# Kernel optimization log

Hardware: AMD Instinct MI355X
Metric: run time of the kernel (lower is better)

## Reference

```python
import jax, jax.numpy as jnp
import numpy as np

B, L, D = 2, 2048, 2048
H, G, E = 16, 4, 128       # num_heads, group_num, head dim
KV = H // G                # kv heads = 4
OUT = D                    # output_dim == input_dim for residual


def setup_inputs() -> dict:
    key = jax.random.key(0)
    ks = jax.random.split(key, 12)
    s_in = 1.0 / np.sqrt(D)
    s_o = 1.0 / np.sqrt(H * E)
    return {
        "x": jax.random.normal(ks[0], (B, L, D), jnp.float32),
        "Wq": jax.random.normal(ks[1], (D, H * E), jnp.float32) * s_in,
        "bq": jnp.zeros((H * E,), jnp.float32),
        "Wk": jax.random.normal(ks[2], (D, KV * E), jnp.float32) * s_in,
        "bk": jnp.zeros((KV * E,), jnp.float32),
        "Wv": jax.random.normal(ks[3], (D, KV * E), jnp.float32) * s_in,
        "bv": jnp.zeros((KV * E,), jnp.float32),
        "Wo": jax.random.normal(ks[4], (H * E, OUT), jnp.float32) * s_o,
        "bo": jnp.zeros((OUT,), jnp.float32),
        "gamma": jnp.ones((OUT,), jnp.float32),
        "beta": jnp.zeros((OUT,), jnp.float32),
    }


def reference(x, Wq, bq, Wk, bk, Wv, bv, Wo, bo, gamma, beta):
    b, l, _ = x.shape
    Q = (x @ Wq + bq).reshape(b, l, H, E)            # [B,L,H,E]
    K = (x @ Wk + bk).reshape(b, l, KV, E)           # [B,L,KV,E]
    V = (x @ Wv + bv).reshape(b, l, KV, E)
    # GQA expand: reshape(B,L,1,KV,E).expand(G) -> head h = g*KV + kv (tile kv heads G times)
    K = jnp.broadcast_to(K[:, :, None, :, :], (b, l, G, KV, E)).reshape(b, l, H, E)
    V = jnp.broadcast_to(V[:, :, None, :, :], (b, l, G, KV, E)).reshape(b, l, H, E)
    scores = jnp.einsum('blhe,bmhe->bhlm', Q, K) / np.sqrt(E).astype(np.float32)
    # causal mask: triu(ones, diag=1) * -1e9 added to scores
    mask = jnp.triu(jnp.ones((l, l), jnp.float32), k=1) * (-1e9)
    attn = jax.nn.softmax(scores + mask[None, None, :, :], axis=-1)
    ctx = jnp.einsum('bhlm,bmhe->blhe', attn, V).reshape(b, l, H * E)
    y = jax.nn.gelu(ctx @ Wo + bo, approximate=False)  # nn.GELU default = exact erf
    r = x + y
    mu = jnp.mean(r, axis=-1, keepdims=True)
    var = jnp.var(r, axis=-1, keepdims=True)
    return (r - mu) * jax.lax.rsqrt(var + 1e-5) * gamma + beta
```

## Files before the change

kernel.cpp:

```cpp
#include <hip/hip_runtime.h>
#include <hip/hip_bf16.h>
#include <math.h>

typedef __bf16 bf16_t;
typedef __bf16 bf16x4 __attribute__((ext_vector_type(4)));
typedef __bf16 bf16x8 __attribute__((ext_vector_type(8)));
typedef float  f32x4  __attribute__((ext_vector_type(4)));
typedef float  f32x16 __attribute__((ext_vector_type(16)));

#define MFMA16(a,b,c) __builtin_amdgcn_mfma_f32_16x16x32_bf16((a),(b),(c),0,0,0)
#define MFMA32(a,b,c) __builtin_amdgcn_mfma_f32_32x32x16_bf16((a),(b),(c),0,0,0)

#define B_ 2
#define L_ 2048
#define D_ 2048
#define H_ 16
#define KV_ 4
#define E_ 128
#define M_ (B_*L_)
#define NQKV_ 3072

__device__ __forceinline__ void async_ld16(const bf16_t* g, bf16_t* l) {
    __builtin_amdgcn_global_load_lds((const __attribute__((address_space(1))) void*)g,
                                     (__attribute__((address_space(3))) void*)l, 16, 0, 0);
}

__global__ __launch_bounds__(256) void cast_bias_kernel(const float* __restrict__ src,
                                                        bf16_t* __restrict__ dst,
                                                        const float* __restrict__ bq,
                                                        const float* __restrict__ bk,
                                                        const float* __restrict__ bv,
                                                        float* __restrict__ qbias) {
    int bid = blockIdx.x;
    if (bid < 8192) {
        int i = (bid * 256 + threadIdx.x) * 4;
        float4 v = *(const float4*)(src + i);
        bf16x4 o;
        o.x = (bf16_t)v.x; o.y = (bf16_t)v.y; o.z = (bf16_t)v.z; o.w = (bf16_t)v.w;
        *(bf16x4*)(dst + i) = o;
    } else {
        int i = (bid - 8192) * 256 + threadIdx.x;
        if (i < 2048) qbias[i] = bq[i];
        else if (i < 2560) qbias[i] = bk[i - 2048];
        else if (i < 3072) qbias[i] = bv[i - 2560];
    }
}

__global__ __launch_bounds__(256) void wtrans_kernel(const float* __restrict__ Wq,
                                                     const float* __restrict__ Wk,
                                                     const float* __restrict__ Wv,
                                                     const float* __restrict__ Wo,
                                                     bf16_t* __restrict__ WqkvT,
                                                     bf16_t* __restrict__ WoT) {
    __shared__ float tile[32][33];
    int bx = blockIdx.x;
    const float* W; bf16_t* WT; int N, n0;
    if (bx < 64)      { W = Wq; WT = WqkvT;                  N = 2048; n0 = bx * 32; }
    else if (bx < 80) { W = Wk; WT = WqkvT + 2048 * 2048;    N = 512;  n0 = (bx - 64) * 32; }
    else if (bx < 96) { W = Wv; WT = WqkvT + 2560 * 2048;    N = 512;  n0 = (bx - 80) * 32; }
    else              { W = Wo; WT = WoT;                    N = 2048; n0 = (bx - 96) * 32; }
    int k0 = blockIdx.y * 32;
    int tx = threadIdx.x, ty = threadIdx.y;
    #pragma unroll
    for (int i = 0; i < 32; i += 8)
        tile[ty + i][tx] = W[(size_t)(k0 + ty + i) * N + n0 + tx];
    __syncthreads();
    #pragma unroll
    for (int i = 0; i < 32; i += 8)
        WT[(size_t)(n0 + ty + i) * 2048 + k0 + tx] = (bf16_t)tile[tx][ty + i];
}

__global__ __launch_bounds__(256) void transpose_v_kernel(const bf16_t* __restrict__ QKV,
                                                          bf16_t* __restrict__ Vt) {
    __shared__ bf16_t tile[32][33];
    int e0 = blockIdx.x * 32, l0 = blockIdx.y * 32;
    int bk = blockIdx.z;
    int b = bk >> 2, kv = bk & 3;
    int tx = threadIdx.x, ty = threadIdx.y;
    #pragma unroll
    for (int i = 0; i < 32; i += 8)
        tile[ty + i][tx] = QKV[(size_t)(b * L_ + l0 + ty + i) * NQKV_ + 2560 + kv * 128 + e0 + tx];
    __syncthreads();
    #pragma unroll
    for (int i = 0; i < 32; i += 8)
        Vt[((size_t)bk * 128 + e0 + ty + i) * L_ + l0 + tx] = tile[tx][ty + i];
}

template <bool OUT_BF16, bool GELU>
__global__ __launch_bounds__(256) void gemm_kernel(const bf16_t* __restrict__ A,
                                                   const bf16_t* __restrict__ BT,
                                                   const float* __restrict__ bias,
                                                   void* __restrict__ C,
                                                   int M, int N, int K) {
    __shared__ __align__(16) bf16_t sA[128][32];
    __shared__ __align__(16) bf16_t sB[128][32];
    int tid = threadIdx.x;
    int wave = tid >> 6, lane = tid & 63;
    int l16 = lane & 15, quad = lane >> 4;
    int row0 = blockIdx.y * 128;
    int col0 = blockIdx.x * 128;
    int wm = (wave >> 1) * 64;
    int wn = (wave & 1) * 64;

    f32x4 acc[4][4];
    #pragma unroll
    for (int i = 0; i < 4; ++i)
        #pragma unroll
        for (int j = 0; j < 4; ++j)
            acc[i][j] = f32x4{0.f, 0.f, 0.f, 0.f};

    for (int k0 = 0; k0 < K; k0 += 32) {
        #pragma unroll
        for (int c = 0; c < 2; ++c) {
            int lin = (c * 256 + tid) * 8;
            int r = lin >> 5, col = lin & 31;
            async_ld16(&A[(size_t)(row0 + r) * K + k0 + col], &sA[r][col]);
            async_ld16(&BT[(size_t)(col0 + r) * K + k0 + col], &sB[r][col]);
        }
        __syncthreads();
        bf16x8 af[4], bf[4];
        #pragma unroll
        for (int mt = 0; mt < 4; ++mt) af[mt] = *(const bf16x8*)&sA[wm + mt * 16 + l16][quad * 8];
        #pragma unroll
        for (int nt = 0; nt < 4; ++nt) bf[nt] = *(const bf16x8*)&sB[wn + nt * 16 + l16][quad * 8];
        #pragma unroll
        for (int mt = 0; mt < 4; ++mt)
            #pragma unroll
            for (int nt = 0; nt < 4; ++nt)
                acc[mt][nt] = MFMA16(af[mt], bf[nt], acc[mt][nt]);
        __syncthreads();
    }

    #pragma unroll
    for (int mt = 0; mt < 4; ++mt) {
        #pragma unroll
        for (int nt = 0; nt < 4; ++nt) {
            int gcol = col0 + wn + nt * 16 + l16;
            float bv = bias[gcol];
            #pragma unroll
            for (int r = 0; r < 4; ++r) {
                int grow = row0 + wm + mt * 16 + quad * 4 + r;
                float v = acc[mt][nt][r] + bv;
                if (GELU) v = 0.5f * v * (1.f + erff(v * 0.70710678118654752f));
                if (OUT_BF16) ((bf16_t*)C)[(size_t)grow * N + gcol] = (bf16_t)v;
                else          ((float*)C)[(size_t)grow * N + gcol] = v;
            }
        }
    }
}

__global__ __launch_bounds__(256) void attn_kernel(const bf16_t* __restrict__ QKV,
                                                   const bf16_t* __restrict__ Vt,
                                                   bf16_t* __restrict__ Ctx) {
    __shared__ __align__(16) bf16_t sK[2][64][128];
    __shared__ __align__(16) bf16_t sV[2][128][64];

    const int tid = threadIdx.x;
    const int wave = tid >> 6, lane = tid & 63;
    const int l31 = lane & 31, half = lane >> 5;

    const int idx = blockIdx.x;
    const int r = idx >> 5;
    const int bh = idx & 31;
    const int t = (r < 8) ? (15 - r) : (r - 8);
    const int h = bh & 15, b = bh >> 4;
    const int kv = h & 3;

    const bf16_t* Kbase = QKV + (size_t)b * L_ * NQKV_ + 2048 + kv * 128;
    const bf16_t* Vbase = Vt + (size_t)(b * 4 + kv) * 128 * L_;
    const float SC = 0.12754995f;

    const int qrow = t * 128 + wave * 32 + l31;
    const int ktlast = 2 * t + 1;
    const int ktmax_w = 2 * t + (wave >> 1);

    bf16x8 qf[8];
    const bf16_t* Qrow = QKV + (size_t)(b * L_ + qrow) * NQKV_ + h * 128 + half * 8;
    #pragma unroll
    for (int et = 0; et < 8; ++et) qf[et] = *(const bf16x8*)&Qrow[et * 16];

    f32x16 acc[4];
    #pragma unroll
    for (int em = 0; em < 4; ++em)
        #pragma unroll
        for (int j = 0; j < 16; ++j) acc[em][j] = 0.f;
    float l_i = 0.f;

    bf16x8 kreg[4], vreg[4];
    #define LOAD_TILE(KT)                                                            \
        {                                                                            \
            int kk = (KT) * 64;                                                      \
            _Pragma("unroll")                                                        \
            for (int p = 0; p < 4; ++p) {                                            \
                int ch = p * 256 + tid;                                              \
                int rk = ch >> 4, ck = ch & 15;                                      \
                kreg[p] = *(const bf16x8*)&Kbase[(size_t)(kk + rk) * NQKV_ + ck * 8];\
                int rv = ch >> 3, cv = ch & 7;                                       \
                vreg[p] = *(const bf16x8*)&Vbase[(size_t)rv * L_ + kk + cv * 8];     \
            }                                                                        \
        }

    LOAD_TILE(0);

    for (int kt = 0; kt <= ktlast; ++kt) {
        const int bufi = kt & 1;
        #pragma unroll
        for (int p = 0; p < 4; ++p) {
            int ch = p * 256 + tid;
            int rk = ch >> 4, ck = ch & 15;
            *(bf16x8*)&sK[bufi][rk][(ck ^ (rk & 15)) * 8] = kreg[p];
            int rv = ch >> 3, cv = ch & 7;
            *(bf16x8*)&sV[bufi][rv][(cv ^ (rv & 7)) * 8] = vreg[p];
        }
        __syncthreads();
        if (kt < ktlast) LOAD_TILE(kt + 1);

        if (kt <= ktmax_w) {
            f32x16 s0[2], s1[2];
            #pragma unroll
            for (int mt = 0; mt < 2; ++mt)
                #pragma unroll
                for (int j = 0; j < 16; ++j) { s0[mt][j] = 0.f; s1[mt][j] = 0.f; }
            __builtin_amdgcn_s_setprio(1);
            #pragma unroll
            for (int mt = 0; mt < 2; ++mt)
                #pragma unroll
                for (int ep = 0; ep < 4; ++ep) {
                    bf16x8 kf0 = *(const bf16x8*)&sK[bufi][mt * 32 + l31][((ep * 4 + half) ^ (l31 & 15)) * 8];
                    bf16x8 kf1 = *(const bf16x8*)&sK[bufi][mt * 32 + l31][((ep * 4 + 2 + half) ^ (l31 & 15)) * 8];
                    s0[mt] = MFMA32(kf0, qf[ep * 2], s0[mt]);
                    s1[mt] = MFMA32(kf1, qf[ep * 2 + 1], s1[mt]);
                }
            __builtin_amdgcn_s_setprio(0);
            f32x16 s[2];
            #pragma unroll
            for (int mt = 0; mt < 2; ++mt)
                #pragma unroll
                for (int j = 0; j < 16; ++j) s[mt][j] = s0[mt][j] + s1[mt][j];

            if (kt == ktmax_w) {
                #pragma unroll
                for (int mt = 0; mt < 2; ++mt)
                    #pragma unroll
                    for (int j = 0; j < 16; ++j) {
                        int kidx = kt * 64 + mt * 32 + (j & 3) + 8 * (j >> 2) + 4 * half;
                        if (kidx > qrow) s[mt][j] = -3.0e38f;
                    }
            }

            float rs = 0.f;
            #pragma unroll
            for (int mt = 0; mt < 2; ++mt)
                #pragma unroll
                for (int j = 0; j < 16; ++j) {
                    float p = exp2f(s[mt][j] * SC);
                    s[mt][j] = p;
                    rs += p;
                }
            rs += __shfl_xor(rs, 32, 64);
            l_i += rs;

            bf16x4 pk[2][4];
            #pragma unroll
            for (int mt = 0; mt < 2; ++mt)
                #pragma unroll
                for (int g = 0; g < 4; ++g) {
                    bf16x4 tt;
                    #pragma unroll
                    for (int i = 0; i < 4; ++i) tt[i] = (bf16_t)s[mt][g * 4 + i];
                    pk[mt][g] = tt;
                }

            #pragma unroll
            for (int kc = 0; kc < 4; ++kc) {
                const int mts = kc >> 1, g0 = 2 * (kc & 1);
                bf16x4 send = half ? pk[mts][g0] : pk[mts][g0 + 1];
                bf16x4 keep = half ? pk[mts][g0 + 1] : pk[mts][g0];
                union { bf16x4 v; int i[2]; } su, ru;
                su.v = send;
                ru.i[0] = __shfl_xor(su.i[0], 32, 64);
                ru.i[1] = __shfl_xor(su.i[1], 32, 64);
                bf16x4 lo = half ? ru.v : keep;
                bf16x4 hi = half ? keep : ru.v;
                bf16x8 pf = __builtin_shufflevector(lo, hi, 0, 1, 2, 3, 4, 5, 6, 7);
                __builtin_amdgcn_s_setprio(1);
                #pragma unroll
                for (int em = 0; em < 4; ++em) {
                    bf16x8 vf = *(const bf16x8*)&sV[bufi][em * 32 + l31][((kc * 2 + half) ^ (l31 & 7)) * 8];
                    acc[em] = MFMA32(vf, pf, acc[em]);
                }
                __builtin_amdgcn_s_setprio(0);
            }
        }
    }

    const float inv = 1.f / l_i;
    bf16_t* Cp = Ctx + (size_t)(b * L_ + qrow) * 2048 + h * 128;
    #pragma unroll
    for (int em = 0; em < 4; ++em)
        #pragma unroll
        for (int g = 0; g < 4; ++g) {
            bf16x4 ov;
            #pragma unroll
            for (int i = 0; i < 4; ++i) ov[i] = (bf16_t)(acc[em][g * 4 + i] * inv);
            *(bf16x4*)&Cp[em * 32 + g * 8 + half * 4] = ov;
        }
}

__global__ __launch_bounds__(256) void ln_kernel(const bf16_t* __restrict__ Y,
                                                 const float* __restrict__ X,
                                                 const float* __restrict__ gamma,
                                                 const float* __restrict__ beta,
                                                 float* __restrict__ out) {
    __shared__ float sr[2048];
    __shared__ float wred[8];
    size_t row = blockIdx.x;
    const bf16_t* y = Y + row * 2048;
    const float* x = X + row * 2048;
    float sum = 0.f, ssq = 0.f;
    #pragma unroll
    for (int c = 0; c < 2; ++c) {
        int i = (c * 256 + threadIdx.x) * 4;
        bf16x4 yv = *(const bf16x4*)(y + i);
        float4 xv = *(const float4*)(x + i);
        float r0 = xv.x + (float)yv[0];
        float r1 = xv.y + (float)yv[1];
        float r2 = xv.z + (float)yv[2];
        float r3 = xv.w + (float)yv[3];
        sr[i] = r0; sr[i + 1] = r1; sr[i + 2] = r2; sr[i + 3] = r3;
        sum += r0 + r1 + r2 + r3;
        ssq += r0 * r0 + r1 * r1 + r2 * r2 + r3 * r3;
    }
    #pragma unroll
    for (int off = 32; off > 0; off >>= 1) {
        sum += __shfl_xor(sum, off, 64);
        ssq += __shfl_xor(ssq, off, 64);
    }
    int wv = threadIdx.x >> 6;
    if ((threadIdx.x & 63) == 0) { wred[wv] = sum; wred[wv + 4] = ssq; }
    __syncthreads();
    sum = wred[0] + wred[1] + wred[2] + wred[3];
    ssq = wred[4] + wred[5] + wred[6] + wred[7];
    float mu = sum * (1.f / 2048.f);
    float var = ssq * (1.f / 2048.f) - mu * mu;
    float rstd = rsqrtf(var + 1e-5f);
    #pragma unroll
    for (int c = 0; c < 2; ++c) {
        int i = (c * 256 + threadIdx.x) * 4;
        float4 gv = *(const float4*)(gamma + i);
        float4 bv = *(const float4*)(beta + i);
        float4 o;
        o.x = (sr[i]     - mu) * rstd * gv.x + bv.x;
        o.y = (sr[i + 1] - mu) * rstd * gv.y + bv.y;
        o.z = (sr[i + 2] - mu) * rstd * gv.z + bv.z;
        o.w = (sr[i + 3] - mu) * rstd * gv.w + bv.w;
        *(float4*)(out + row * 2048 + i) = o;
    }
}

extern "C" void kernel_launch(void* const* d_in, const int* in_sizes, int n_in,
                              void* d_out, int out_size, void* d_ws, size_t ws_size,
                              hipStream_t stream) {
    const float* x     = (const float*)d_in[0];
    const float* Wq    = (const float*)d_in[1];
    const float* bq    = (const float*)d_in[2];
    const float* Wk    = (const float*)d_in[3];
    const float* bk    = (const float*)d_in[4];
    const float* Wv    = (const float*)d_in[5];
    const float* bv    = (const float*)d_in[6];
    const float* Wo    = (const float*)d_in[7];
    const float* bo    = (const float*)d_in[8];
    const float* gamma = (const float*)d_in[9];
    const float* beta  = (const float*)d_in[10];
    float* out = (float*)d_out;

    char* ws = (char*)d_ws;
    size_t off = 0;
    bf16_t* xb    = (bf16_t*)(ws + off); off += 16777216;
    bf16_t* WqkvT = (bf16_t*)(ws + off); off += 12582912;
    bf16_t* WoT   = (bf16_t*)(ws + off); off += 8388608;
    float*  qbias = (float*)(ws + off);  off += 12288;
    bf16_t* QKV   = (bf16_t*)(ws + off); off += 25165824;
    bf16_t* Vt    = (bf16_t*)(ws + off); off += 4194304;
    bf16_t* Cb    = (bf16_t*)(ws + off); off += 16777216;
    bf16_t* Yb    = (bf16_t*)(ws + off); off += 16777216;

    cast_bias_kernel<<<8204, 256, 0, stream>>>(x, xb, bq, bk, bv, qbias);
    wtrans_kernel<<<dim3(160, 64), dim3(32, 8), 0, stream>>>(Wq, Wk, Wv, Wo, WqkvT, WoT);

    gemm_kernel<true, false><<<dim3(24, 32), 256, 0, stream>>>(xb, WqkvT, qbias, QKV, M_, NQKV_, D_);
    transpose_v_kernel<<<dim3(4, 64, 8), dim3(32, 8), 0, stream>>>(QKV, Vt);
    attn_kernel<<<512, 256, 0, stream>>>(QKV, Vt, Cb);
    gemm_kernel<true, true><<<dim3(16, 32), 256, 0, stream>>>(Cb, WoT, bo, Yb, M_, D_, 2048);
    ln_kernel<<<M_, 256, 0, stream>>>(Yb, x, gamma, beta, out);
}
```

Baseline: 387.0 us.

## Restructure attention into 64-row blocks with async K staging and direct V loads

The attention kernel now runs 1024 blocks of 128 threads, each covering 64 query rows instead of 128, with a new tile ordering that pairs long and short causal rows for load balance. K tiles are staged into LDS through asynchronous global-to-LDS loads. V fragments are read straight from global memory into registers, so the V shared buffer goes away. This removes the wasted diagonal work of idle waves and the register round-trip for staging, but adds per-wave global V traffic and higher register pressure.

```diff
diff --git a/kernel.cpp b/kernel.cpp
--- a/kernel.cpp
+++ b/kernel.cpp
@@ -149,20 +149,19 @@
     }
 }
 
-__global__ __launch_bounds__(256) void attn_kernel(const bf16_t* __restrict__ QKV,
-                                                   const bf16_t* __restrict__ Vt,
-                                                   bf16_t* __restrict__ Ctx) {
+__global__ __launch_bounds__(128, 2) void attn_kernel(const bf16_t* __restrict__ QKV,
+                                                      const bf16_t* __restrict__ Vt,
+                                                      bf16_t* __restrict__ Ctx) {
     __shared__ __align__(16) bf16_t sK[2][64][128];
-    __shared__ __align__(16) bf16_t sV[2][128][64];
 
     const int tid = threadIdx.x;
     const int wave = tid >> 6, lane = tid & 63;
     const int l31 = lane & 31, half = lane >> 5;
 
     const int idx = blockIdx.x;
-    const int r = idx >> 5;
+    const int rr = idx >> 5;
     const int bh = idx & 31;
-    const int t = (r < 8) ? (15 - r) : (r - 8);
+    const int u = (rr < 8) ? 31 - rr : (rr < 16) ? rr - 8 : (rr < 24) ? 39 - rr : rr - 16;
     const int h = bh & 15, b = bh >> 4;
     const int kv = h & 3;
 
@@ -170,9 +169,7 @@
     const bf16_t* Vbase = Vt + (size_t)(b * 4 + kv) * 128 * L_;
     const float SC = 0.12754995f;
 
-    const int qrow = t * 128 + wave * 32 + l31;
-    const int ktlast = 2 * t + 1;
-    const int ktmax_w = 2 * t + (wave >> 1);
+    const int qrow = u * 64 + wave * 32 + l31;
 
     bf16x8 qf[8];
     const bf16_t* Qrow = QKV + (size_t)(b * L_ + qrow) * NQKV_ + h * 128 + half * 8;
@@ -186,112 +183,109 @@
         for (int j = 0; j < 16; ++j) acc[em][j] = 0.f;
     float l_i = 0.f;
 
-    bf16x8 kreg[4], vreg[4];
-    #define LOAD_TILE(KT)                                                            \
-        {                                                                            \
-            int kk = (KT) * 64;                                                      \
-            _Pragma("unroll")                                                        \
-            for (int p = 0; p < 4; ++p) {                                            \
-                int ch = p * 256 + tid;                                              \
-                int rk = ch >> 4, ck = ch & 15;                                      \
-                kreg[p] = *(const bf16x8*)&Kbase[(size_t)(kk + rk) * NQKV_ + ck * 8];\
-                int rv = ch >> 3, cv = ch & 7;                                       \
-                vreg[p] = *(const bf16x8*)&Vbase[(size_t)rv * L_ + kk + cv * 8];     \
-            }                                                                        \
-        }
-
-    LOAD_TILE(0);
-
-    for (int kt = 0; kt <= ktlast; ++kt) {
+    #define STAGE_K(KT, BUF)                                                          \
+        {                                                                             \
+            int kk = (KT) * 64;                                                       \
+            _Pragma("unroll")                                                         \
+            for (int rep = 0; rep < 8; ++rep) {                                       \
+                int ch = rep * 128 + tid;                                             \
+                int rk = ch >> 4;                                                     \
+                int sc = (ch & 15) ^ (rk & 15);                                       \
+                async_ld16(&Kbase[(size_t)(kk + rk) * NQKV_ + sc * 8],                \
+                           ((bf16_t*)sK[BUF]) + (size_t)ch * 8);                      \
+            }                                                                         \
+        }
+
+    STAGE_K(0, 0);
+    __syncthreads();
+
+    for (int kt = 0; kt <= u; ++kt) {
         const int bufi = kt & 1;
-        #pragma unroll
-        for (int p = 0; p < 4; ++p) {
-            int ch = p * 256 + tid;
-            int rk = ch >> 4, ck = ch & 15;
-            *(bf16x8*)&sK[bufi][rk][(ck ^ (rk & 15)) * 8] = kreg[p];
-            int rv = ch >> 3, cv = ch & 7;
-            *(bf16x8*)&sV[bufi][rv][(cv ^ (rv & 7)) * 8] = vreg[p];
-        }
-        __syncthreads();
-        if (kt < ktlast) LOAD_TILE(kt + 1);
-
-        if (kt <= ktmax_w) {
-            f32x16 s0[2], s1[2];
-            #pragma unroll
-            for (int mt = 0; mt < 2; ++mt)
-                #pragma unroll
-                for (int j = 0; j < 16; ++j) { s0[mt][j] = 0.f; s1[mt][j] = 0.f; }
-            __builtin_amdgcn_s_setprio(1);
-            #pragma unroll
-            for (int mt = 0; mt < 2; ++mt)
-                #pragma unroll
-                for (int ep = 0; ep < 4; ++ep) {
-                    bf16x8 kf0 = *(const bf16x8*)&sK[bufi][mt * 32 + l31][((ep * 4 + half) ^ (l31 & 15)) * 8];
-                    bf16x8 kf1 = *(const bf16x8*)&sK[bufi][mt * 32 + l31][((ep * 4 + 2 + half) ^ (l31 & 15)) * 8];
-                    s0[mt] = MFMA32(kf0, qf[ep * 2], s0[mt]);
-                    s1[mt] = MFMA32(kf1, qf[ep * 2 + 1], s1[mt]);
-                }
-            __builtin_amdgcn_s_setprio(0);
-            f32x16 s[2];
-            #pragma unroll
-            for (int mt = 0; mt < 2; ++mt)
-                #pragma unroll
-                for (int j = 0; j < 16; ++j) s[mt][j] = s0[mt][j] + s1[mt][j];
-
-            if (kt == ktmax_w) {
-                #pragma unroll
-                for (int mt = 0; mt < 2; ++mt)
-                    #pragma unroll
-                    for (int j = 0; j < 16; ++j) {
-                        int kidx = kt * 64 + mt * 32 + (j & 3) + 8 * (j >> 2) + 4 * half;
-                        if (kidx > qrow) s[mt][j] = -3.0e38f;
-                    }
+        if (kt < u) STAGE_K(kt + 1, bufi ^ 1);
+
+        bf16x8 vr[16];
+        #pragma unroll
+        for (int kc = 0; kc < 2; ++kc)
+            #pragma unroll
+            for (int em = 0; em < 4; ++em)
+                vr[kc * 4 + em] = *(const bf16x8*)&Vbase[(size_t)(em * 32 + l31) * L_ +
+                                                         kt * 64 + (kc * 2 + half) * 8];
+
+        f32x16 s[2];
+        #pragma unroll
+        for (int mt = 0; mt < 2; ++mt)
+            #pragma unroll
+            for (int j = 0; j < 16; ++j) s[mt][j] = 0.f;
+        __builtin_amdgcn_s_setprio(1);
+        #pragma unroll
+        for (int mt = 0; mt < 2; ++mt)
+            #pragma unroll
+            for (int et = 0; et < 8; ++et) {
+                bf16x8 kf = *(const bf16x8*)&sK[bufi][mt * 32 + l31][((et * 2 + half) ^ (l31 & 15)) * 8];
+                s[mt] = MFMA32(kf, qf[et], s[mt]);
             }
-
-            float rs = 0.f;
+        __builtin_amdgcn_s_setprio(0);
+
+        #pragma unroll
+        for (int kc = 2; kc < 4; ++kc)
+            #pragma unroll
+            for (int em = 0; em < 4; ++em)
+                vr[kc * 4 + em] = *(const bf16x8*)&Vbase[(size_t)(em * 32 + l31) * L_ +
+                                                         kt * 64 + (kc * 2 + half) * 8];
+
+        if (kt == u) {
             #pragma unroll
             for (int mt = 0; mt < 2; ++mt)
                 #pragma unroll
                 for (int j = 0; j < 16; ++j) {
-                    float p = exp2f(s[mt][j] * SC);
-                    s[mt][j] = p;
-                    rs += p;
+                    int kidx = kt * 64 + mt * 32 + (j & 3) + 8 * (j >> 2) + 4 * half;
+                    if (kidx > qrow) s[mt][j] = -3.0e38f;
                 }
-            rs += __shfl_xor(rs, 32, 64);
-            l_i += rs;
-
-            bf16x4 pk[2][4];
-            #pragma unroll
-            for (int mt = 0; mt < 2; ++mt)
+        }
+
+        float rs = 0.f;
+        #pragma unroll
+        for (int mt = 0; mt < 2; ++mt)
+            #pragma unroll
+            for (int j = 0; j < 16; ++j) {
+                float p = exp2f(s[mt][j] * SC);
+                s[mt][j] = p;
+                rs += p;
+            }
+        rs += __shfl_xor(rs, 32, 64);
+        l_i += rs;
+
+        bf16x4 pk[2][4];
+        #pragma unroll
+        for (int mt = 0; mt < 2; ++mt)
+            #pragma unroll
+            for (int g = 0; g < 4; ++g) {
+                bf16x4 tt;
                 #pragma unroll
-                for (int g = 0; g < 4; ++g) {
-                    bf16x4 tt;
-                    #pragma unroll
-                    for (int i = 0; i < 4; ++i) tt[i] = (bf16_t)s[mt][g * 4 + i];
-                    pk[mt][g] = tt;
-                }
-
-            #pragma unroll
-            for (int kc = 0; kc < 4; ++kc) {
-                const int mts = kc >> 1, g0 = 2 * (kc & 1);
-                bf16x4 send = half ? pk[mts][g0] : pk[mts][g0 + 1];
-                bf16x4 keep = half ? pk[mts][g0 + 1] : pk[mts][g0];
-                union { bf16x4 v; int i[2]; } su, ru;
-                su.v = send;
-                ru.i[0] = __shfl_xor(su.i[0], 32, 64);
-                ru.i[1] = __shfl_xor(su.i[1], 32, 64);
-                bf16x4 lo = half ? ru.v : keep;
-                bf16x4 hi = half ? keep : ru.v;
-                bf16x8 pf = __builtin_shufflevector(lo, hi, 0, 1, 2, 3, 4, 5, 6, 7);
-                __builtin_amdgcn_s_setprio(1);
-                #pragma unroll
-                for (int em = 0; em < 4; ++em) {
-                    bf16x8 vf = *(const bf16x8*)&sV[bufi][em * 32 + l31][((kc * 2 + half) ^ (l31 & 7)) * 8];
-                    acc[em] = MFMA32(vf, pf, acc[em]);
-                }
-                __builtin_amdgcn_s_setprio(0);
+                for (int i = 0; i < 4; ++i) tt[i] = (bf16_t)s[mt][g * 4 + i];
+                pk[mt][g] = tt;
             }
-        }
+
+        #pragma unroll
+        for (int kc = 0; kc < 4; ++kc) {
+            const int mts = kc >> 1, g0 = 2 * (kc & 1);
+            bf16x4 send = half ? pk[mts][g0] : pk[mts][g0 + 1];
+            bf16x4 keep = half ? pk[mts][g0 + 1] : pk[mts][g0];
+            union { bf16x4 v; int i[2]; } su, ru;
+            su.v = send;
+            ru.i[0] = __shfl_xor(su.i[0], 32, 64);
+            ru.i[1] = __shfl_xor(su.i[1], 32, 64);
+            bf16x4 lo = half ? ru.v : keep;
+            bf16x4 hi = half ? keep : ru.v;
+            bf16x8 pf = __builtin_shufflevector(lo, hi, 0, 1, 2, 3, 4, 5, 6, 7);
+            __builtin_amdgcn_s_setprio(1);
+            #pragma unroll
+            for (int em = 0; em < 4; ++em)
+                acc[em] = MFMA32(vr[kc * 4 + em], pf, acc[em]);
+            __builtin_amdgcn_s_setprio(0);
+        }
+
+        __syncthreads();
     }
 
     const float inv = 1.f / l_i;
@@ -390,7 +384,7 @@
 
     gemm_kernel<true, false><<<dim3(24, 32), 256, 0, stream>>>(xb, WqkvT, qbias, QKV, M_, NQKV_, D_);
     transpose_v_kernel<<<dim3(4, 64, 8), dim3(32, 8), 0, stream>>>(QKV, Vt);
-    attn_kernel<<<512, 256, 0, stream>>>(QKV, Vt, Cb);
+    attn_kernel<<<1024, 128, 0, stream>>>(QKV, Vt, Cb);
     gemm_kernel<true, true><<<dim3(16, 32), 256, 0, stream>>>(Cb, WoT, bo, Yb, M_, D_, 2048);
     ln_kernel<<<M_, 256, 0, stream>>>(Yb, x, gamma, beta, out);
 }
```

After: 358.7 us. 1.08x faster.
